# Kernel optimization log

Measured on AMD Instinct MI355X. Metric: run time of the kernel, lower is better.

Reference implementation:

```python
import jax, jax.numpy as jnp
import numpy as np

T, B, D_IN, D_H, D_OUT = 128, 256, 256, 1024, 256


def _rand_orth(dim, seed=0):
    rng = np.random.default_rng(seed)
    q, _ = np.linalg.qr(rng.normal(size=(dim, dim)))
    return jnp.asarray(q, dtype=jnp.float32)


def setup_inputs() -> dict:
    key = jax.random.key(0)
    k_xs, k_w1x, k_w2 = jax.random.split(key, 3)
    return {
        "xs": jax.random.normal(k_xs, (T, B, D_IN), dtype=jnp.float32),
        "W1x": 0.1 * jax.random.normal(k_w1x, (D_IN, D_H), dtype=jnp.float32),
        "W1h": _rand_orth(D_H),
        "b1": jnp.zeros((D_H,), dtype=jnp.float32),
        "W2": 0.1 * jax.random.normal(k_w2, (D_H, D_OUT), dtype=jnp.float32),
        "b2": jnp.zeros((), dtype=jnp.float32),
    }


def reference(xs, W1x, W1h, b1, W2, b2):
    # xs: [T, B, D_in]; tanh-RNN recurrence over time, then linear readout.
    h0 = jnp.zeros((xs.shape[1], W1h.shape[0]), dtype=xs.dtype)

    def step(h, x):
        h = jnp.tanh(x @ W1x + h @ W1h + b1)
        return h, None

    h, _ = jax.lax.scan(step, h0, xs)
    return h @ W2 + b2
```

## Files before the change

### kernel.cpp

```cpp
#include <hip/hip_runtime.h>
#include <hip/hip_bf16.h>
#include <math.h>

#define TT   128
#define BB   256
#define DIN  256
#define DH   1024
#define DOUT 256

#define NGM 8
#define MR  32
#define NGN 32
#define NC  32

typedef float  floatx4 __attribute__((ext_vector_type(4)));
typedef short  shortx8 __attribute__((ext_vector_type(8)));
typedef unsigned long long u64;

#define CMASK 0x0001000100010001ULL
#define GSTRIDE 32768

__device__ __forceinline__ short f2bf(float f) {
    union { float f; unsigned u; } v; v.f = f;
    unsigned r = v.u + 0x7fffu + ((v.u >> 16) & 1u);
    return (short)(r >> 16);
}

__device__ __forceinline__ unsigned short bf15e(float v, unsigned bit) {
    union { float f; unsigned u; } x; x.f = v;
    unsigned ua = x.u - (bit << 16);
    unsigned k  = (ua + 0xFFFFu + ((ua >> 17) & 1u)) >> 17;
    return (unsigned short)((k << 1) | bit);
}

__device__ __forceinline__ shortx8 mk8(u64 lo, u64 hi) {
    union { struct { u64 a, b; } s; shortx8 v; } u;
    u.s.a = lo; u.s.b = hi;
    return u.v;
}

__device__ __forceinline__ float fast_tanh(float z) {
    float e = __expf(2.0f * fabsf(z));
    float r = 1.0f - 2.0f / (e + 1.0f);
    return copysignf(r, z);
}

#define AGLD(p)    __hip_atomic_load((p),  __ATOMIC_RELAXED, __HIP_MEMORY_SCOPE_AGENT)
#define AGST(p, v) __hip_atomic_store((p), (v), __ATOMIC_RELAXED, __HIP_MEMORY_SCOPE_AGENT)

#define LD16(buf, base) do { \
    _Pragma("unroll") \
    for (int _j = 0; _j < 8; ++_j) { \
        const u64* _p = (const u64*)(hfr + ((base) + _j) * 512); \
        buf[2 * _j]     = AGLD(_p); \
        buf[2 * _j + 1] = AGLD(_p + 1); \
    } } while (0)
#define OK16(buf, okvar) do { \
    int _o = 1; \
    _Pragma("unroll") \
    for (int _j = 0; _j < 16; ++_j) _o &= ((buf[_j] & CMASK) == pat); \
    okvar = __all(_o); } while (0)
#define WAITVALID(buf, base) do { \
    int _okk; OK16(buf, _okk); \
    while (!_okk) { __builtin_amdgcn_s_sleep(1); LD16(buf, base); OK16(buf, _okk); } \
    } while (0)
#define CONS16(buf, base) do { \
    _Pragma("unroll") \
    for (int _j = 0; _j < 8; ++_j) { \
        shortx8 bfr = mk8(buf[2 * _j], buf[2 * _j + 1]); \
        shortx8 a0 = *(const shortx8*)&WhL[(base) + _j][0][q][lr][0]; \
        shortx8 a1 = *(const shortx8*)&WhL[(base) + _j][1][q][lr][0]; \
        acc0 = __builtin_amdgcn_mfma_f32_16x16x32_bf16(a0, bfr, acc0, 0, 0, 0); \
        acc1 = __builtin_amdgcn_mfma_f32_16x16x32_bf16(a1, bfr, acc1, 0, 0, 0); \
    } } while (0)

__global__ __launch_bounds__(128, 1) void rnn_steps_kernel(
    const float* __restrict__ xs, const float* __restrict__ W1x,
    const float* __restrict__ W1h, const float* __restrict__ b1,
    short* __restrict__ Hbuf)
{
    const int gm  = blockIdx.x;
    const int gn  = blockIdx.y;
    const int tid = threadIdx.x;
    const int w   = tid >> 6;
    const int l   = tid & 63;
    const int lr  = l & 15;
    const int q   = l >> 4;

    const int r0 = gm * MR;
    const int c0 = gn * NC;

    __shared__ short WhL[DH / 32][2][4][16][8];
    for (int idx = tid; idx < (DH / 32) * 2 * 4 * 16; idx += 128) {
        const int c  = idx & 15;
        const int qq = (idx >> 4) & 3;
        const int ct = (idx >> 6) & 1;
        const int ks = idx >> 7;
        shortx8 f;
        #pragma unroll
        for (int j = 0; j < 8; ++j)
            f[j] = f2bf(W1h[(size_t)(ks * 32 + qq * 8 + j) * DH + c0 + ct * 16 + c]);
        *(shortx8*)&WhL[ks][ct][qq][c][0] = f;
    }
    shortx8 wx[2][8];
    #pragma unroll
    for (int ct = 0; ct < 2; ++ct)
        #pragma unroll
        for (int ks = 0; ks < 8; ++ks) {
            shortx8 f;
            #pragma unroll
            for (int j = 0; j < 8; ++j)
                f[j] = f2bf(W1x[(size_t)(ks * 32 + q * 8 + j) * DH + c0 + ct * 16 + lr]);
            wx[ct][ks] = f;
        }
    __syncthreads();

    floatx4 bias[2];
    #pragma unroll
    for (int ct = 0; ct < 2; ++ct)
        #pragma unroll
        for (int r = 0; r < 4; ++r) bias[ct][r] = b1[c0 + ct * 16 + q * 4 + r];

    const int myrow = r0 + w * 16 + lr;
    const size_t HS = (size_t)BB * DH;

    short* const Hg   = Hbuf + gm * GSTRIDE;
    const int rdoff   = w * 16384 + q * 128 + lr * 8;
    const int wroff   = w * 16384 + gn * 512 + (q >> 1) * 128 + lr * 8 + (q & 1) * 4;

    for (int t = 1; t <= TT; ++t) {
        const short* const hfr = Hg + (size_t)((t - 1) & 1) * HS + rdoff;
        const int pc = (t >= 2) ? (1 + ((t - 2) % 15)) : 0;
        const u64 pat = ((u64)(pc & 1)) | ((u64)((pc >> 1) & 1) << 16) |
                        ((u64)((pc >> 2) & 1) << 32) | ((u64)((pc >> 3) & 1) << 48);

        u64 A[16], B[16];
        if (t > 1) LD16(A, 0);

        floatx4 acc0 = {0.f, 0.f, 0.f, 0.f}, acc1 = {0.f, 0.f, 0.f, 0.f};

        {
            const float* xrow = xs + ((size_t)(t - 1) * BB + myrow) * DIN + q * 8;
            #pragma unroll
            for (int ks = 0; ks < 8; ++ks) {
                floatx4 x0 = *(const floatx4*)(xrow + ks * 32);
                floatx4 x1 = *(const floatx4*)(xrow + ks * 32 + 4);
                shortx8 b;
                b[0] = f2bf(x0[0]); b[1] = f2bf(x0[1]); b[2] = f2bf(x0[2]); b[3] = f2bf(x0[3]);
                b[4] = f2bf(x1[0]); b[5] = f2bf(x1[1]); b[6] = f2bf(x1[2]); b[7] = f2bf(x1[3]);
                acc0 = __builtin_amdgcn_mfma_f32_16x16x32_bf16(wx[0][ks], b, acc0, 0, 0, 0);
                acc1 = __builtin_amdgcn_mfma_f32_16x16x32_bf16(wx[1][ks], b, acc1, 0, 0, 0);
            }
        }

        if (t > 1) {
            LD16(B, 8);
            WAITVALID(A, 0);  CONS16(A, 0);
            LD16(A, 16);
            WAITVALID(B, 8);  CONS16(B, 8);
            LD16(B, 24);
            WAITVALID(A, 16); CONS16(A, 16);
            WAITVALID(B, 24); CONS16(B, 24);
        }

        {
            const int cc = 1 + ((t - 1) % 15);
            short* hp = Hg + (size_t)(t & 1) * HS + wroff;
            u64 p0 = 0, p1 = 0;
            #pragma unroll
            for (int r = 0; r < 4; ++r) {
                const unsigned bit = ((unsigned)cc >> r) & 1u;
                p0 |= ((u64)bf15e(fast_tanh(acc0[r] + bias[0][r]), bit)) << (16 * r);
                p1 |= ((u64)bf15e(fast_tanh(acc1[r] + bias[1][r]), bit)) << (16 * r);
            }
            AGST((u64*)(hp), p0);
            AGST((u64*)(hp + 256), p1);
        }
    }
}

__global__ __launch_bounds__(256) void readout_kernel(
    const short* __restrict__ Hfin, const float* __restrict__ W2,
    const float* __restrict__ b2, float* __restrict__ out)
{
    const int o  = threadIdx.x;
    const int b0 = blockIdx.x * 4;
    __shared__ u64 hs8[4 * DH / 4];
    for (int ch = o; ch < 4 * DH / 4; ch += 256) {
        const int row  = ch >> 8;
        const int col0 = (ch & 255) * 4;
        const int rr   = b0 + row;
        const int gmr  = rr >> 5, rt = (rr >> 4) & 1, lrr = rr & 15;
        const int ks   = col0 >> 5, qq = (col0 >> 3) & 3, j0 = col0 & 7;
        const u64* src = (const u64*)(Hfin + (size_t)gmr * GSTRIDE + rt * 16384 +
                                      ks * 512 + qq * 128 + lrr * 8 + j0);
        hs8[ch] = AGLD(src);
    }
    __syncthreads();
    const unsigned* h0 = (const unsigned*)&hs8[0 * 256];
    const unsigned* h1 = (const unsigned*)&hs8[1 * 256];
    const unsigned* h2 = (const unsigned*)&hs8[2 * 256];
    const unsigned* h3 = (const unsigned*)&hs8[3 * 256];
    float a0 = 0.f, a1 = 0.f, a2 = 0.f, a3 = 0.f;
    for (int k2 = 0; k2 < DH / 2; ++k2) {
        float w0 = W2[(2 * k2)     * DOUT + o];
        float w1 = W2[(2 * k2 + 1) * DOUT + o];
        unsigned p0 = h0[k2], p1 = h1[k2], p2 = h2[k2], p3 = h3[k2];
        a0 += __builtin_bit_cast(float, p0 << 16) * w0 + __builtin_bit_cast(float, p0 & 0xffff0000u) * w1;
        a1 += __builtin_bit_cast(float, p1 << 16) * w0 + __builtin_bit_cast(float, p1 & 0xffff0000u) * w1;
        a2 += __builtin_bit_cast(float, p2 << 16) * w0 + __builtin_bit_cast(float, p2 & 0xffff0000u) * w1;
        a3 += __builtin_bit_cast(float, p3 << 16) * w0 + __builtin_bit_cast(float, p3 & 0xffff0000u) * w1;
    }
    const float bias = b2[0];
    out[(b0 + 0) * DOUT + o] = a0 + bias;
    out[(b0 + 1) * DOUT + o] = a1 + bias;
    out[(b0 + 2) * DOUT + o] = a2 + bias;
    out[(b0 + 3) * DOUT + o] = a3 + bias;
}

extern "C" void kernel_launch(void* const* d_in, const int* in_sizes, int n_in,
                              void* d_out, int out_size, void* d_ws, size_t ws_size,
                              hipStream_t stream) {
    (void)in_sizes; (void)n_in; (void)out_size; (void)ws_size;
    const float* xs  = (const float*)d_in[0];
    const float* W1x = (const float*)d_in[1];
    const float* W1h = (const float*)d_in[2];
    const float* b1  = (const float*)d_in[3];
    const float* W2  = (const float*)d_in[4];
    const float* b2  = (const float*)d_in[5];
    float* out = (float*)d_out;

    short* Hbuf = (short*)d_ws;

    rnn_steps_kernel<<<dim3(NGM, NGN), 128, 0, stream>>>(xs, W1x, W1h, b1, Hbuf);
    readout_kernel<<<dim3(BB / 4), 256, 0, stream>>>(Hbuf, W2, b2, out);
}
```

Measured before the change: 753.3 us.

## Issue all hidden-state loads upfront, consume chunks out of order, prefetch next xs

Each step now issues all four hidden-state chunk loads at once and polls them in a loop, consuming whichever chunk has become valid instead of waiting on them in a fixed order. The MFMA accumulation is split into two independent accumulator pairs that are summed at the end, which shortens the dependency chain. The next timestep's xs rows are prefetched into registers during the current step so their global loads are off the critical path. In exchange, register pressure rises (four 16-entry u64 buffers plus 16 floatx4 of xs), and the polling loop has more branching.

```diff
diff --git a/kernel.cpp b/kernel.cpp
--- a/kernel.cpp
+++ b/kernel.cpp
@@ -60,18 +60,14 @@
     _Pragma("unroll") \
     for (int _j = 0; _j < 16; ++_j) _o &= ((buf[_j] & CMASK) == pat); \
     okvar = __all(_o); } while (0)
-#define WAITVALID(buf, base) do { \
-    int _okk; OK16(buf, _okk); \
-    while (!_okk) { __builtin_amdgcn_s_sleep(1); LD16(buf, base); OK16(buf, _okk); } \
-    } while (0)
-#define CONS16(buf, base) do { \
+#define CONS16(buf, base, accX, accY) do { \
     _Pragma("unroll") \
     for (int _j = 0; _j < 8; ++_j) { \
         shortx8 bfr = mk8(buf[2 * _j], buf[2 * _j + 1]); \
         shortx8 a0 = *(const shortx8*)&WhL[(base) + _j][0][q][lr][0]; \
         shortx8 a1 = *(const shortx8*)&WhL[(base) + _j][1][q][lr][0]; \
-        acc0 = __builtin_amdgcn_mfma_f32_16x16x32_bf16(a0, bfr, acc0, 0, 0, 0); \
-        acc1 = __builtin_amdgcn_mfma_f32_16x16x32_bf16(a1, bfr, acc1, 0, 0, 0); \
+        accX = __builtin_amdgcn_mfma_f32_16x16x32_bf16(a0, bfr, accX, 0, 0, 0); \
+        accY = __builtin_amdgcn_mfma_f32_16x16x32_bf16(a1, bfr, accY, 0, 0, 0); \
     } } while (0)
 
 __global__ __launch_bounds__(128, 1) void rnn_steps_kernel(
@@ -128,42 +124,73 @@
     const int rdoff   = w * 16384 + q * 128 + lr * 8;
     const int wroff   = w * 16384 + gn * 512 + (q >> 1) * 128 + lr * 8 + (q & 1) * 4;
 
+    floatx4 xf[16];
+    {
+        const float* xrow = xs + (size_t)myrow * DIN + q * 8;
+        #pragma unroll
+        for (int ks = 0; ks < 8; ++ks) {
+            xf[2 * ks]     = *(const floatx4*)(xrow + ks * 32);
+            xf[2 * ks + 1] = *(const floatx4*)(xrow + ks * 32 + 4);
+        }
+    }
+
     for (int t = 1; t <= TT; ++t) {
         const short* const hfr = Hg + (size_t)((t - 1) & 1) * HS + rdoff;
         const int pc = (t >= 2) ? (1 + ((t - 2) % 15)) : 0;
         const u64 pat = ((u64)(pc & 1)) | ((u64)((pc >> 1) & 1) << 16) |
                         ((u64)((pc >> 2) & 1) << 32) | ((u64)((pc >> 3) & 1) << 48);
 
-        u64 A[16], B[16];
-        if (t > 1) LD16(A, 0);
-
-        floatx4 acc0 = {0.f, 0.f, 0.f, 0.f}, acc1 = {0.f, 0.f, 0.f, 0.f};
-
-        {
-            const float* xrow = xs + ((size_t)(t - 1) * BB + myrow) * DIN + q * 8;
+        u64 bA[16], bB[16], bC[16], bD[16];
+        if (t > 1) { LD16(bA, 0); LD16(bB, 8); LD16(bC, 16); LD16(bD, 24); }
+
+        floatx4 accA0 = {0.f, 0.f, 0.f, 0.f}, accA1 = {0.f, 0.f, 0.f, 0.f};
+        floatx4 accB0 = {0.f, 0.f, 0.f, 0.f}, accB1 = {0.f, 0.f, 0.f, 0.f};
+
+        #pragma unroll
+        for (int ks = 0; ks < 8; ++ks) {
+            floatx4 x0 = xf[2 * ks], x1 = xf[2 * ks + 1];
+            shortx8 b;
+            b[0] = f2bf(x0[0]); b[1] = f2bf(x0[1]); b[2] = f2bf(x0[2]); b[3] = f2bf(x0[3]);
+            b[4] = f2bf(x1[0]); b[5] = f2bf(x1[1]); b[6] = f2bf(x1[2]); b[7] = f2bf(x1[3]);
+            accA0 = __builtin_amdgcn_mfma_f32_16x16x32_bf16(wx[0][ks], b, accA0, 0, 0, 0);
+            accA1 = __builtin_amdgcn_mfma_f32_16x16x32_bf16(wx[1][ks], b, accA1, 0, 0, 0);
+        }
+
+        if (t < TT) {
+            const float* xrow = xs + ((size_t)t * BB + myrow) * DIN + q * 8;
             #pragma unroll
             for (int ks = 0; ks < 8; ++ks) {
-                floatx4 x0 = *(const floatx4*)(xrow + ks * 32);
-                floatx4 x1 = *(const floatx4*)(xrow + ks * 32 + 4);
-                shortx8 b;
-                b[0] = f2bf(x0[0]); b[1] = f2bf(x0[1]); b[2] = f2bf(x0[2]); b[3] = f2bf(x0[3]);
-                b[4] = f2bf(x1[0]); b[5] = f2bf(x1[1]); b[6] = f2bf(x1[2]); b[7] = f2bf(x1[3]);
-                acc0 = __builtin_amdgcn_mfma_f32_16x16x32_bf16(wx[0][ks], b, acc0, 0, 0, 0);
-                acc1 = __builtin_amdgcn_mfma_f32_16x16x32_bf16(wx[1][ks], b, acc1, 0, 0, 0);
+                xf[2 * ks]     = *(const floatx4*)(xrow + ks * 32);
+                xf[2 * ks + 1] = *(const floatx4*)(xrow + ks * 32 + 4);
             }
         }
 
         if (t > 1) {
-            LD16(B, 8);
-            WAITVALID(A, 0);  CONS16(A, 0);
-            LD16(A, 16);
-            WAITVALID(B, 8);  CONS16(B, 8);
-            LD16(B, 24);
-            WAITVALID(A, 16); CONS16(A, 16);
-            WAITVALID(B, 24); CONS16(B, 24);
+            int done = 0;
+            while (done != 0xF) {
+                if (!(done & 1)) {
+                    int ok; OK16(bA, ok);
+                    if (ok) { CONS16(bA, 0, accA0, accA1); done |= 1; } else LD16(bA, 0);
+                }
+                if (!(done & 2)) {
+                    int ok; OK16(bB, ok);
+                    if (ok) { CONS16(bB, 8, accB0, accB1); done |= 2; } else LD16(bB, 8);
+                }
+                if (!(done & 4)) {
+                    int ok; OK16(bC, ok);
+                    if (ok) { CONS16(bC, 16, accA0, accA1); done |= 4; } else LD16(bC, 16);
+                }
+                if (!(done & 8)) {
+                    int ok; OK16(bD, ok);
+                    if (ok) { CONS16(bD, 24, accB0, accB1); done |= 8; } else LD16(bD, 24);
+                }
+                if (done != 0xF) __builtin_amdgcn_s_sleep(1);
+            }
         }
 
         {
+            const floatx4 acc0 = accA0 + accB0;
+            const floatx4 acc1 = accA1 + accB1;
             const int cc = 1 + ((t - 1) % 15);
             short* hp = Hg + (size_t)(t & 1) * HS + wroff;
             u64 p0 = 0, p1 = 0;
```

Result: slower. 1.038 ms (+37.8%).
